# Kernel tuning notes

Measured on AMD Instinct MI355X. Metric: run time of the kernel, lower is better.

The kernel has to match this reference:

```python
import jax, jax.numpy as jnp
import numpy as np

B, Nq, C, H = 1, 300, 256, 8
h, w = 32, 32
HW = h * w
HID = 512  # rpe_hidden_dim
HD = C // H


def setup_inputs() -> dict:
    key = jax.random.key(0)
    ks = jax.random.split(key, 16)
    s = 0.02
    inp = {
        "raw_query": jax.random.normal(ks[0], (B, Nq, C), jnp.float32),
        "query_pos": jax.random.normal(ks[1], (B, Nq, C), jnp.float32),
        "reference_points": jax.random.uniform(ks[2], (B, Nq, 2), jnp.float32),
        "raw_src": jax.random.normal(ks[3], (B, HW, C), jnp.float32),
        "src_pos_embed": jax.random.normal(ks[4], (B, HW, C), jnp.float32),
        "Wq": jax.random.normal(ks[5], (C, C), jnp.float32) * s,
        "bq": jnp.zeros((C,), jnp.float32),
        "Wk": jax.random.normal(ks[6], (C, C), jnp.float32) * s,
        "bk": jnp.zeros((C,), jnp.float32),
        "Wv": jax.random.normal(ks[7], (C, C), jnp.float32) * s,
        "bv": jnp.zeros((C,), jnp.float32),
        "Wo": jax.random.normal(ks[8], (C, C), jnp.float32) * s,
        "bo": jnp.zeros((C,), jnp.float32),
        "W1": jax.random.normal(ks[9], (HID, 2), jnp.float32),   # cpb MLP layer 1
        "b1": jnp.zeros((HID,), jnp.float32),
        "W2": jax.random.normal(ks[10], (H, HID), jnp.float32) * s,  # cpb MLP layer 2 (no bias)
        "input_spatial_shapes": np.array([[h, w]], dtype=np.int64),
    }
    return inp


def _key_positions(hh, ww):
    ys = (jnp.arange(hh, dtype=jnp.float32) + 0.5) / hh
    xs = (jnp.arange(ww, dtype=jnp.float32) + 0.5) / ww
    yy, xx = jnp.meshgrid(ys, xs, indexing="ij")  # row-major: idx = y*w + x
    return jnp.stack([xx.ravel(), yy.ravel()], axis=-1)  # [HW, 2] (x, y)


def reference(raw_query, query_pos, reference_points, raw_src, src_pos_embed,
              Wq, bq, Wk, bk, Wv, bv, Wo, bo, W1, b1, W2, input_spatial_shapes):
    hh, ww = int(input_spatial_shapes[0, 0]), int(input_spatial_shapes[0, 1])
    scale = HD ** (-0.5)
    queries = raw_query + query_pos                      # [B,Nq,C]
    memory = raw_src + src_pos_embed                     # [B,HW,C]

    q = (queries @ Wq.T + bq).reshape(B, Nq, H, HD)
    k = (memory @ Wk.T + bk).reshape(B, hh * ww, H, HD)
    v = (memory @ Wv.T + bv).reshape(B, hh * ww, H, HD)

    logits = jnp.einsum("bqhd,bkhd->bhqk", q, k) * scale  # [B,H,Nq,HW]

    key_pos = _key_positions(hh, ww)                      # [HW,2]
    delta = reference_points[:, :, None, :] - key_pos[None, None]  # [B,Nq,HW,2]
    hid = jax.nn.relu(jnp.einsum("bqkc,hc->bqkh", delta, W1) + b1)  # [B,Nq,HW,HID]
    bias = jnp.einsum("bqkf,hf->bhqk", hid, W2)           # [B,H,Nq,HW]

    attn = jax.nn.softmax(logits + bias, axis=-1)
    out = jnp.einsum("bhqk,bkhd->bqhd", attn, v).reshape(B, Nq, C)
    return out @ Wo.T + bo
```

## Files before the change

### kernel.cpp

```cpp
#include <hip/hip_runtime.h>
#include <hip/hip_fp16.h>
#include <stdint.h>

#define NQ   300
#define CDIM 256
#define NH   8
#define HD   32
#define HWK  1024
#define HIDD 512

typedef __attribute__((ext_vector_type(8))) _Float16 f16x8;
typedef __attribute__((ext_vector_type(2))) _Float16 h2v;
typedef __attribute__((ext_vector_type(4))) float f32x4;

#define QB_OFF   0
#define KB_OFF   153600
#define VT_OFF   677888
#define PO_OFF   1202176
#define PL_OFF   3659776
#define A16_OFF  3736576
#define NX_OFF   4043776
#define NY_OFF   4044800
#define W2_OFF   4045824

__device__ __forceinline__ short f16b(float x){
  _Float16 h = (_Float16)x;
  return __builtin_bit_cast(short, h);
}

__device__ __forceinline__ uint32_t pk_f16(float a, float b){
  auto r = __builtin_amdgcn_cvt_pkrtz(a, b);
  return __builtin_bit_cast(uint32_t, r);
}

__global__ __launch_bounds__(256) void prep_kernel(
    const float* __restrict__ refp, const float* __restrict__ W1,
    const float* __restrict__ b1, const float* __restrict__ W2,
    short* __restrict__ a16, short* __restrict__ nx16,
    short* __restrict__ ny16, short* __restrict__ w216)
{
  int idx = blockIdx.x * 256 + threadIdx.x;
  if (idx < NQ*HIDD){
    int q = idx >> 9, f = idx & 511;
    float2 w = ((const float2*)W1)[f];
    float a = fmaf(w.x, refp[2*q], fmaf(w.y, refp[2*q+1], b1[f]));
    a16[idx] = f16b(a);
  } else {
    int j = idx - NQ*HIDD;
    if (j < HIDD){
      float2 w = ((const float2*)W1)[j];
      nx16[j] = f16b(-w.x);
      ny16[j] = f16b(-w.y);
    } else if (j < HIDD + NH*HIDD){
      int e = j - HIDD;
      w216[e] = f16b(W2[e]);
    }
  }
}

__global__ __launch_bounds__(256) void proj_kernel(
    const float* __restrict__ rq, const float* __restrict__ qp,
    const float* __restrict__ rs, const float* __restrict__ spe,
    const float* __restrict__ Wq, const float* __restrict__ bq,
    const float* __restrict__ Wk, const float* __restrict__ bk,
    const float* __restrict__ Wv, const float* __restrict__ bv,
    const float* __restrict__ Wo, const float* __restrict__ bo,
    char* __restrict__ ws, float* __restrict__ dout, int final_mode)
{
  int bxid = blockIdx.x;
  int tile = bxid >> 1, half = bxid & 1;
  const float *in1, *in2, *W, *bias;
  int r0, M, mode;
  const float* po = (const float*)(ws + PO_OFF);
  const float* pl = (const float*)(ws + PL_OFF);
  if (final_mode){
    in1 = po; in2 = nullptr; W = Wo; bias = bo;
    r0 = tile*16; M = NQ; mode = 3;
  } else if (tile < 19){
    in1 = rq; in2 = qp; W = Wq; bias = bq; r0 = tile*16; M = NQ; mode = 0;
  } else if (tile < 83){
    in1 = rs; in2 = spe; W = Wk; bias = bk; r0 = (tile-19)*16; M = HWK; mode = 1;
  } else {
    in1 = rs; in2 = spe; W = Wv; bias = bv; r0 = (tile-83)*16; M = HWK; mode = 2;
  }
  __shared__ __align__(16) float At[32][20];
  __shared__ float Wl[32][129];
  __shared__ float linv[16][8];
  int tid = threadIdx.x;
  int n_loc = tid & 127;
  int rg = tid >> 7;
  int n = half*128 + n_loc;
  float acc[8];
  float bv_ = bias[n];
  #pragma unroll
  for (int i=0;i<8;i++) acc[i] = bv_;

  if (mode == 3 && tid < 128){
    int r = tid >> 3, hh = tid & 7;
    int gr = r0 + r; if (gr >= M) gr = M - 1;
    float s = 0.f;
    #pragma unroll
    for (int p = 0; p < 8; p++) s += pl[((size_t)p*NQ+gr)*NH+hh];
    linv[r][hh] = 1.0f / s;
  }

  for (int c0 = 0; c0 < CDIM; c0 += 32){
    __syncthreads();
    for (int e = tid; e < 512; e += 256){
      int r = e >> 5, c = e & 31;
      int gr = r0 + r; if (gr >= M) gr = M - 1;
      float v;
      if (mode == 3){
        int cc = c0 + c;
        v = 0.f;
        #pragma unroll
        for (int p = 0; p < 8; p++) v += po[(size_t)(p*NQ+gr)*CDIM + cc];
        v *= linv[r][c0 >> 5];
      } else {
        v = in1[gr*CDIM + c0 + c];
        if (in2) v += in2[gr*CDIM + c0 + c];
      }
      At[c][r] = v;
    }
    for (int e = tid; e < 4096; e += 256){
      int c = e & 31, nn = e >> 5;
      Wl[c][nn] = W[(half*128 + nn)*CDIM + c0 + c];
    }
    __syncthreads();
    #pragma unroll
    for (int c = 0; c < 32; c++){
      float w = Wl[c][n_loc];
      const float4* ap = (const float4*)&At[c][rg*8];
      float4 a0 = ap[0], a1 = ap[1];
      acc[0] = fmaf(a0.x, w, acc[0]);
      acc[1] = fmaf(a0.y, w, acc[1]);
      acc[2] = fmaf(a0.z, w, acc[2]);
      acc[3] = fmaf(a0.w, w, acc[3]);
      acc[4] = fmaf(a1.x, w, acc[4]);
      acc[5] = fmaf(a1.y, w, acc[5]);
      acc[6] = fmaf(a1.z, w, acc[6]);
      acc[7] = fmaf(a1.w, w, acc[7]);
    }
  }

  if (mode == 0){
    short* qb = (short*)(ws + QB_OFF);
    const float s = 0.17677669529663687f;
    #pragma unroll
    for (int i=0;i<8;i++){
      int gr = r0 + rg*8 + i;
      if (gr < M) qb[gr*CDIM + n] = f16b(acc[i]*s);
    }
  } else if (mode == 1){
    short* kb = (short*)(ws + KB_OFF);
    int h = n >> 5, d = n & 31;
    #pragma unroll
    for (int i=0;i<8;i++){
      int gr = r0 + rg*8 + i;
      if (gr < M) kb[((size_t)h*HWK + gr)*HD + d] = f16b(acc[i]);
    }
  } else if (mode == 2){
    short* vt = (short*)(ws + VT_OFF);
    uint32_t p[4];
    #pragma unroll
    for (int i=0;i<4;i++) p[i] = pk_f16(acc[2*i], acc[2*i+1]);
    *(uint4*)(vt + n*HWK + r0 + rg*8) = make_uint4(p[0], p[1], p[2], p[3]);
  } else {
    #pragma unroll
    for (int i=0;i<8;i++){
      int gr = r0 + rg*8 + i;
      if (gr < M) dout[gr*CDIM + n] = acc[i];
    }
  }
}

__global__ __launch_bounds__(256, 5) void fused_kernel(
    const short* __restrict__ a16, const short* __restrict__ nx16,
    const short* __restrict__ ny16, const short* __restrict__ w216,
    const short* __restrict__ qb, const short* __restrict__ kb,
    const short* __restrict__ vt, float* __restrict__ po,
    float* __restrict__ pl)
{
  int bid = blockIdx.x;
  int q = bid >> 3, kr = bid & 7;
  int tid = threadIdx.x, wave = tid >> 6, lane = tid & 63;
  int n = lane & 15, qd = lane >> 4;

  __shared__ __align__(16) _Float16 nwx[HIDD];
  __shared__ __align__(16) _Float16 c1s[4][HIDD];
  __shared__ __align__(16) _Float16 w2l[NH][520];
  __shared__ __align__(16) _Float16 pb[NH][136];
  __shared__ __align__(16) float part[4][NH][32];
  __shared__ float lsum[4][NH];

  {
    int f0 = tid * 2;
    h2v a2 = *(const h2v*)(a16 + q*HIDD + f0);
    h2v ny2 = *(const h2v*)(ny16 + f0);
    h2v nx2 = *(const h2v*)(nx16 + f0);
    *(h2v*)&nwx[f0] = nx2;
    #pragma unroll
    for (int r = 0; r < 4; r++){
      _Float16 kyh = (_Float16)(((float)(kr*4 + r) + 0.5f) * (1.0f/32.0f));
      h2v ky2 = {kyh, kyh};
      *(h2v*)&c1s[r][f0] = ny2 * ky2 + a2;
    }
  }
  for (int e = tid; e < 512; e += 256){
    int r = e >> 6, c = e & 63;
    *(f16x8*)&w2l[r][c*8] = *(const f16x8*)(w216 + r*HIDD + c*8);
  }
  f16x8 qfrag;
  if (n < NH) qfrag = *(const f16x8*)(qb + q*CDIM + n*HD + qd*8);
  else { f16x8 z = {0,0,0,0,0,0,0,0}; qfrag = z; }
  f16x8 qm[NH];
  #pragma unroll
  for (int h = 0; h < NH; h++){
    f16x8 z = {0,0,0,0,0,0,0,0};
    qm[h] = (n == h) ? qfrag : z;
  }
  __syncthreads();

  const int kyrow = kr*4 + wave;
  const int kbase = kyrow * 32;

  f32x4 acc[2];
  #pragma unroll
  for (int t = 0; t < 2; t++){
    int k0 = kbase + t*16;
    f32x4 d = {0.f,0.f,0.f,0.f};
    #pragma unroll
    for (int h = 0; h < NH; h++){
      f16x8 af = *(const f16x8*)(kb + ((size_t)h*HWK + k0 + n)*HD + qd*8);
      d = __builtin_amdgcn_mfma_f32_16x16x32_f16(af, qm[h], d, 0, 0, 0);
    }
    acc[t] = d;
  }

  _Float16 kxAh = (_Float16)(((float)n + 0.5f) * (1.0f/32.0f));
  _Float16 kxBh = (_Float16)(((float)n + 16.5f) * (1.0f/32.0f));
  f16x8 kxA8, kxB8, z8;
  #pragma unroll
  for (int j = 0; j < 8; j++){ kxA8[j] = kxAh; kxB8[j] = kxBh; z8[j] = (_Float16)0.f; }
  const _Float16* c1r = &c1s[wave][0];
  #pragma unroll 4
  for (int kc = 0; kc < 16; kc++){
    int f0 = kc*32 + qd*8;
    f16x8 c1v = *(const f16x8*)(c1r + f0);
    f16x8 wxv = *(const f16x8*)(&nwx[f0]);
    f16x8 bfr = *(const f16x8*)(&w2l[n & 7][f0]);
    #pragma unroll
    for (int t = 0; t < 2; t++){
      f16x8 kx8 = t ? kxB8 : kxA8;
      f16x8 e = __builtin_elementwise_max(wxv * kx8 + c1v, z8);
      acc[t] = __builtin_amdgcn_mfma_f32_16x16x32_f16(e, bfr, acc[t], 0, 0, 0);
    }
  }

  float lacc = 0.f;
  #pragma unroll
  for (int t = 0; t < 2; t++){
    float e0 = __expf(acc[t][0]);
    float e1 = __expf(acc[t][1]);
    float e2 = __expf(acc[t][2]);
    float e3 = __expf(acc[t][3]);
    if (n < NH){
      uint2 p2;
      p2.x = pk_f16(e0, e1);
      p2.y = pk_f16(e2, e3);
      *(uint2*)&pb[n][wave*32 + t*16 + qd*4] = p2;
    }
    float s = e0 + e1 + e2 + e3;
    s += __shfl_xor(s, 16);
    s += __shfl_xor(s, 32);
    lacc += s;
  }
  if (lane < NH) lsum[wave][lane] = lacc;

  #pragma unroll
  for (int h = 0; h < NH; h++){
    int kl = wave*32 + qd*8;
    f16x8 pa = *(const f16x8*)&pb[h][kl];
    f16x8 v0 = *(const f16x8*)(vt + ((size_t)(h*HD +      n))*HWK + kr*128 + kl);
    f16x8 v1 = *(const f16x8*)(vt + ((size_t)(h*HD + 16 + n))*HWK + kr*128 + kl);
    f32x4 o0 = {0.f,0.f,0.f,0.f}, o1 = {0.f,0.f,0.f,0.f};
    o0 = __builtin_amdgcn_mfma_f32_16x16x32_f16(pa, v0, o0, 0, 0, 0);
    o1 = __builtin_amdgcn_mfma_f32_16x16x32_f16(pa, v1, o1, 0, 0, 0);
    if (qd == 0){
      part[wave][h][n]      = o0[0];
      part[wave][h][16 + n] = o1[0];
    }
  }
  __syncthreads();

  {
    int h = tid >> 5, d = tid & 31;
    float s = part[0][h][d] + part[1][h][d] + part[2][h][d] + part[3][h][d];
    po[((size_t)kr*NQ + q)*CDIM + tid] = s;
    if (tid < NH)
      pl[((size_t)kr*NQ + q)*NH + tid] =
          lsum[0][tid] + lsum[1][tid] + lsum[2][tid] + lsum[3][tid];
  }
}

extern "C" void kernel_launch(void* const* d_in, const int* in_sizes, int n_in,
                              void* d_out, int out_size, void* d_ws, size_t ws_size,
                              hipStream_t stream)
{
  const float* rq  = (const float*)d_in[0];
  const float* qp  = (const float*)d_in[1];
  const float* rp  = (const float*)d_in[2];
  const float* rs  = (const float*)d_in[3];
  const float* spe = (const float*)d_in[4];
  const float* Wq  = (const float*)d_in[5];
  const float* bq  = (const float*)d_in[6];
  const float* Wk  = (const float*)d_in[7];
  const float* bk  = (const float*)d_in[8];
  const float* Wv  = (const float*)d_in[9];
  const float* bv  = (const float*)d_in[10];
  const float* Wo  = (const float*)d_in[11];
  const float* bo  = (const float*)d_in[12];
  const float* W1  = (const float*)d_in[13];
  const float* b1  = (const float*)d_in[14];
  const float* W2  = (const float*)d_in[15];
  char* ws = (char*)d_ws;
  float* dout = (float*)d_out;

  prep_kernel<<<618, 256, 0, stream>>>(rp, W1, b1, W2,
      (short*)(ws + A16_OFF), (short*)(ws + NX_OFF),
      (short*)(ws + NY_OFF), (short*)(ws + W2_OFF));
  proj_kernel<<<294, 256, 0, stream>>>(rq, qp, rs, spe, Wq, bq, Wk, bk,
      Wv, bv, Wo, bo, ws, dout, 0);
  fused_kernel<<<2400, 256, 0, stream>>>((const short*)(ws + A16_OFF),
      (const short*)(ws + NX_OFF), (const short*)(ws + NY_OFF),
      (const short*)(ws + W2_OFF), (const short*)(ws + QB_OFF),
      (const short*)(ws + KB_OFF), (const short*)(ws + VT_OFF),
      (float*)(ws + PO_OFF), (float*)(ws + PL_OFF));
  proj_kernel<<<38, 256, 0, stream>>>(rq, qp, rs, spe, Wq, bq, Wk, bk,
      Wv, bv, Wo, bo, ws, dout, 1);
}
```

Measured before the change: 167.1 us.

## Merge prep into projection kernel, precompute masked Q tiles, raise fused occupancy

The separate prep launch is folded into the projection kernel as extra blocks, removing one launch and its serialization. The projection is retiled into quarters of 64 output columns, giving more blocks. The Q projection now also writes a zero-padded per-head masked Q layout, so the fused kernel loads ready-made MFMA B fragments instead of building eight masked copies in registers. The fused kernel shares one LDS buffer between c1s and part and raises launch bounds to 8 blocks per CU. The trade-off is extra global writes for the zeroed Q tiles and more register pressure under the higher occupancy target.

New measurement: 171.9 us. 2.9% more time.

```diff
diff --git a/kernel.cpp b/kernel.cpp
--- a/kernel.cpp
+++ b/kernel.cpp
@@ -22,6 +22,7 @@
 #define NX_OFF   4043776
 #define NY_OFF   4044800
 #define W2_OFF   4045824
+#define QZ_OFF   4054016
 
 __device__ __forceinline__ short f16b(float x){
   _Float16 h = (_Float16)x;
@@ -33,29 +34,9 @@
   return __builtin_bit_cast(uint32_t, r);
 }
 
-__global__ __launch_bounds__(256) void prep_kernel(
-    const float* __restrict__ refp, const float* __restrict__ W1,
-    const float* __restrict__ b1, const float* __restrict__ W2,
-    short* __restrict__ a16, short* __restrict__ nx16,
-    short* __restrict__ ny16, short* __restrict__ w216)
-{
-  int idx = blockIdx.x * 256 + threadIdx.x;
-  if (idx < NQ*HIDD){
-    int q = idx >> 9, f = idx & 511;
-    float2 w = ((const float2*)W1)[f];
-    float a = fmaf(w.x, refp[2*q], fmaf(w.y, refp[2*q+1], b1[f]));
-    a16[idx] = f16b(a);
-  } else {
-    int j = idx - NQ*HIDD;
-    if (j < HIDD){
-      float2 w = ((const float2*)W1)[j];
-      nx16[j] = f16b(-w.x);
-      ny16[j] = f16b(-w.y);
-    } else if (j < HIDD + NH*HIDD){
-      int e = j - HIDD;
-      w216[e] = f16b(W2[e]);
-    }
-  }
+__device__ __forceinline__ h2v cvt2h(float a, float b){
+  auto r = __builtin_amdgcn_cvt_pkrtz(a, b);
+  return __builtin_bit_cast(h2v, r);
 }
 
 __global__ __launch_bounds__(256) void proj_kernel(
@@ -64,25 +45,247 @@
     const float* __restrict__ Wq, const float* __restrict__ bq,
     const float* __restrict__ Wk, const float* __restrict__ bk,
     const float* __restrict__ Wv, const float* __restrict__ bv,
-    const float* __restrict__ Wo, const float* __restrict__ bo,
-    char* __restrict__ ws, float* __restrict__ dout, int final_mode)
+    const float* __restrict__ refp, const float* __restrict__ W1,
+    const float* __restrict__ b1, const float* __restrict__ W2,
+    char* __restrict__ ws)
 {
   int bxid = blockIdx.x;
-  int tile = bxid >> 1, half = bxid & 1;
+  int tid = threadIdx.x;
+
+  if (bxid >= 588){
+    int pidx = (bxid - 588)*256 + tid;
+    if (pidx < 153600){
+      int q = pidx >> 9, f = pidx & 511;
+      float2 w = ((const float2*)W1)[f];
+      float a = fmaf(w.x, refp[2*q], fmaf(w.y, refp[2*q+1], b1[f]));
+      ((short*)(ws + A16_OFF))[pidx] = f16b(a);
+    } else if (pidx < 154112){
+      int f = pidx - 153600;
+      float2 w = ((const float2*)W1)[f];
+      ((short*)(ws + NX_OFF))[f] = f16b(-w.x);
+      ((short*)(ws + NY_OFF))[f] = f16b(-w.y);
+    } else if (pidx < 158208){
+      int e = pidx - 154112;
+      ((short*)(ws + W2_OFF))[e] = f16b(W2[e]);
+    } else if (pidx < 302208){
+      int z = pidx - 158208;
+      int g = z >> 2, p = z & 3;
+      int q = g / 120, r = g - q*120;
+      int h = r / 15,  m = r - h*15;
+      int n = m + (m >= h ? 1 : 0);
+      f16x8 z8 = {0,0,0,0,0,0,0,0};
+      *(f16x8*)((short*)(ws + QZ_OFF) + (((q*NH + h)*16 + n) << 5) + p*8) = z8;
+    }
+    return;
+  }
+
+  int tile = bxid >> 2, quarter = bxid & 3;
   const float *in1, *in2, *W, *bias;
   int r0, M, mode;
-  const float* po = (const float*)(ws + PO_OFF);
-  const float* pl = (const float*)(ws + PL_OFF);
-  if (final_mode){
-    in1 = po; in2 = nullptr; W = Wo; bias = bo;
-    r0 = tile*16; M = NQ; mode = 3;
-  } else if (tile < 19){
+  if (tile < 19){
     in1 = rq; in2 = qp; W = Wq; bias = bq; r0 = tile*16; M = NQ; mode = 0;
   } else if (tile < 83){
     in1 = rs; in2 = spe; W = Wk; bias = bk; r0 = (tile-19)*16; M = HWK; mode = 1;
   } else {
     in1 = rs; in2 = spe; W = Wv; bias = bv; r0 = (tile-83)*16; M = HWK; mode = 2;
   }
+  __shared__ __align__(16) float At[32][20];
+  __shared__ float Wl[32][68];
+  int nq = tid & 63;
+  int rg = tid >> 6;
+  int n = quarter*64 + nq;
+  float acc[4];
+  float bv_ = bias[n];
+  #pragma unroll
+  for (int i=0;i<4;i++) acc[i] = bv_;
+
+  for (int c0 = 0; c0 < CDIM; c0 += 32){
+    __syncthreads();
+    for (int e = tid; e < 512; e += 256){
+      int r = e >> 5, c = e & 31;
+      int gr = r0 + r; if (gr >= M) gr = M - 1;
+      float v = in1[gr*CDIM + c0 + c];
+      if (in2) v += in2[gr*CDIM + c0 + c];
+      At[c][r] = v;
+    }
+    for (int e = tid; e < 2048; e += 256){
+      int c = e & 31, nn = e >> 5;
+      Wl[c][nn] = W[(quarter*64 + nn)*CDIM + c0 + c];
+    }
+    __syncthreads();
+    #pragma unroll
+    for (int c = 0; c < 32; c++){
+      float w = Wl[c][nq];
+      float4 a = *(const float4*)&At[c][rg*4];
+      acc[0] = fmaf(a.x, w, acc[0]);
+      acc[1] = fmaf(a.y, w, acc[1]);
+      acc[2] = fmaf(a.z, w, acc[2]);
+      acc[3] = fmaf(a.w, w, acc[3]);
+    }
+  }
+
+  if (mode == 0){
+    short* qb = (short*)(ws + QB_OFF);
+    short* qz = (short*)(ws + QZ_OFF);
+    const float s = 0.17677669529663687f;
+    int h = n >> 5, d = n & 31;
+    #pragma unroll
+    for (int i=0;i<4;i++){
+      int gr = r0 + rg*4 + i;
+      if (gr < M){
+        short v = f16b(acc[i]*s);
+        qb[gr*CDIM + n] = v;
+        qz[(((gr*NH + h)*16 + h) << 5) + d] = v;
+      }
+    }
+  } else if (mode == 1){
+    short* kb = (short*)(ws + KB_OFF);
+    int h = n >> 5, d = n & 31;
+    #pragma unroll
+    for (int i=0;i<4;i++){
+      int gr = r0 + rg*4 + i;
+      if (gr < M) kb[((size_t)h*HWK + gr)*HD + d] = f16b(acc[i]);
+    }
+  } else {
+    short* vt = (short*)(ws + VT_OFF);
+    uint2 p2;
+    p2.x = pk_f16(acc[0], acc[1]);
+    p2.y = pk_f16(acc[2], acc[3]);
+    *(uint2*)(vt + n*HWK + r0 + rg*4) = p2;
+  }
+}
+
+__global__ __launch_bounds__(256, 8) void fused_kernel(
+    const short* __restrict__ a16, const short* __restrict__ nx16,
+    const short* __restrict__ ny16, const short* __restrict__ w216,
+    const short* __restrict__ qz, const short* __restrict__ kb,
+    const short* __restrict__ vt, float* __restrict__ po,
+    float* __restrict__ pl)
+{
+  int bid = blockIdx.x;
+  int q = bid >> 3, kr = bid & 7;
+  int tid = threadIdx.x, wave = tid >> 6, lane = tid & 63;
+  int n = lane & 15, qd = lane >> 4;
+
+  __shared__ __align__(16) _Float16 nwx[HIDD];
+  __shared__ __align__(16) char pool[4096];
+  __shared__ __align__(16) _Float16 w2l[NH][520];
+  __shared__ __align__(16) _Float16 pb[NH][136];
+  __shared__ float lsum[4][NH];
+  _Float16 (*c1s)[HIDD] = (_Float16 (*)[HIDD])pool;
+  float (*part)[NH][32] = (float (*)[NH][32])pool;
+
+  {
+    int f0 = tid * 2;
+    h2v a2  = *(const h2v*)(a16 + q*HIDD + f0);
+    h2v ny2 = *(const h2v*)(ny16 + f0);
+    h2v nx2 = *(const h2v*)(nx16 + f0);
+    *(h2v*)&nwx[f0] = nx2;
+    #pragma unroll
+    for (int r = 0; r < 4; r++){
+      _Float16 kyh = (_Float16)(((float)(kr*4 + r) + 0.5f) * (1.0f/32.0f));
+      h2v ky2 = {kyh, kyh};
+      *(h2v*)&c1s[r][f0] = ny2 * ky2 + a2;
+    }
+  }
+  for (int e = tid; e < 512; e += 256){
+    int r = e >> 6, c = e & 63;
+    *(f16x8*)&w2l[r][c*8] = *(const f16x8*)(w216 + r*HIDD + c*8);
+  }
+  __syncthreads();
+
+  const int kyrow = kr*4 + wave;
+  const int kbase = kyrow * 32;
+
+  const short* qzq = qz + q*(NH*16*32);
+  int loff = (n << 5) + qd*8;
+  f32x4 acc[2] = {{0.f,0.f,0.f,0.f},{0.f,0.f,0.f,0.f}};
+  #pragma unroll
+  for (int h = 0; h < NH; h++){
+    f16x8 bq_ = *(const f16x8*)(qzq + (h << 9) + loff);
+    #pragma unroll
+    for (int t = 0; t < 2; t++){
+      int k0 = kbase + t*16;
+      f16x8 af = *(const f16x8*)(kb + ((size_t)h*HWK + k0 + n)*HD + qd*8);
+      acc[t] = __builtin_amdgcn_mfma_f32_16x16x32_f16(af, bq_, acc[t], 0, 0, 0);
+    }
+  }
+
+  _Float16 kxAh = (_Float16)(((float)n + 0.5f) * (1.0f/32.0f));
+  _Float16 kxBh = (_Float16)(((float)n + 16.5f) * (1.0f/32.0f));
+  f16x8 kxA8, kxB8, z8;
+  #pragma unroll
+  for (int j = 0; j < 8; j++){ kxA8[j] = kxAh; kxB8[j] = kxBh; z8[j] = (_Float16)0.f; }
+  const _Float16* c1r = &c1s[wave][0];
+  #pragma unroll 4
+  for (int kc = 0; kc < 16; kc++){
+    int f0 = kc*32 + qd*8;
+    f16x8 c1v = *(const f16x8*)(c1r + f0);
+    f16x8 wxv = *(const f16x8*)(&nwx[f0]);
+    f16x8 bfr = *(const f16x8*)(&w2l[n & 7][f0]);
+    #pragma unroll
+    for (int t = 0; t < 2; t++){
+      f16x8 kx8 = t ? kxB8 : kxA8;
+      f16x8 e = __builtin_elementwise_max(wxv * kx8 + c1v, z8);
+      acc[t] = __builtin_amdgcn_mfma_f32_16x16x32_f16(e, bfr, acc[t], 0, 0, 0);
+    }
+  }
+
+  float lacc = 0.f;
+  #pragma unroll
+  for (int t = 0; t < 2; t++){
+    float e0 = __expf(acc[t][0]);
+    float e1 = __expf(acc[t][1]);
+    float e2 = __expf(acc[t][2]);
+    float e3 = __expf(acc[t][3]);
+    if (n < NH){
+      uint2 p2;
+      p2.x = pk_f16(e0, e1);
+      p2.y = pk_f16(e2, e3);
+      *(uint2*)&pb[n][wave*32 + t*16 + qd*4] = p2;
+    }
+    float s = e0 + e1 + e2 + e3;
+    s += __shfl_xor(s, 16);
+    s += __shfl_xor(s, 32);
+    lacc += s;
+  }
+  if (lane < NH) lsum[wave][lane] = lacc;
+
+  #pragma unroll
+  for (int h = 0; h < NH; h++){
+    int kl = wave*32 + qd*8;
+    f16x8 pa = *(const f16x8*)&pb[h][kl];
+    f16x8 v0 = *(const f16x8*)(vt + ((size_t)(h*HD +      n))*HWK + kr*128 + kl);
+    f16x8 v1 = *(const f16x8*)(vt + ((size_t)(h*HD + 16 + n))*HWK + kr*128 + kl);
+    f32x4 o0 = {0.f,0.f,0.f,0.f}, o1 = {0.f,0.f,0.f,0.f};
+    o0 = __builtin_amdgcn_mfma_f32_16x16x32_f16(pa, v0, o0, 0, 0, 0);
+    o1 = __builtin_amdgcn_mfma_f32_16x16x32_f16(pa, v1, o1, 0, 0, 0);
+    if (qd == 0){
+      part[wave][h][n]      = o0[0];
+      part[wave][h][16 + n] = o1[0];
+    }
+  }
+  __syncthreads();
+
+  {
+    int h = tid >> 5, d = tid & 31;
+    float s = part[0][h][d] + part[1][h][d] + part[2][h][d] + part[3][h][d];
+    po[((size_t)kr*NQ + q)*CDIM + tid] = s;
+    if (tid < NH)
+      pl[((size_t)kr*NQ + q)*NH + tid] =
+          lsum[0][tid] + lsum[1][tid] + lsum[2][tid] + lsum[3][tid];
+  }
+}
+
+__global__ __launch_bounds__(256) void projf_kernel(
+    const float* __restrict__ Wo, const float* __restrict__ bo,
+    char* __restrict__ ws, float* __restrict__ dout)
+{
+  int bxid = blockIdx.x;
+  int tile = bxid >> 1, half = bxid & 1;
+  const float* po = (const float*)(ws + PO_OFF);
+  const float* pl = (const float*)(ws + PL_OFF);
+  int r0 = tile*16, M = NQ;
   __shared__ __align__(16) float At[32][20];
   __shared__ float Wl[32][129];
   __shared__ float linv[16][8];
@@ -91,11 +294,11 @@
   int rg = tid >> 7;
   int n = half*128 + n_loc;
   float acc[8];
-  float bv_ = bias[n];
+  float bv_ = bo[n];
   #pragma unroll
   for (int i=0;i<8;i++) acc[i] = bv_;
 
-  if (mode == 3 && tid < 128){
+  if (tid < 128){
     int r = tid >> 3, hh = tid & 7;
     int gr = r0 + r; if (gr >= M) gr = M - 1;
     float s = 0.f;
@@ -109,22 +312,15 @@
     for (int e = tid; e < 512; e += 256){
       int r = e >> 5, c = e & 31;
       int gr = r0 + r; if (gr >= M) gr = M - 1;
-      float v;
-      if (mode == 3){
-        int cc = c0 + c;
-        v = 0.f;
-        #pragma unroll
-        for (int p = 0; p < 8; p++) v += po[(size_t)(p*NQ+gr)*CDIM + cc];
-        v *= linv[r][c0 >> 5];
-      } else {
-        v = in1[gr*CDIM + c0 + c];
-        if (in2) v += in2[gr*CDIM + c0 + c];
-      }
-      At[c][r] = v;
+      int cc = c0 + c;
+      float v = 0.f;
+      #pragma unroll
+      for (int p = 0; p < 8; p++) v += po[(size_t)(p*NQ+gr)*CDIM + cc];
+      At[c][r] = v * linv[r][c0 >> 5];
     }
     for (int e = tid; e < 4096; e += 256){
       int c = e & 31, nn = e >> 5;
-      Wl[c][nn] = W[(half*128 + nn)*CDIM + c0 + c];
+      Wl[c][nn] = Wo[(half*128 + nn)*CDIM + c0 + c];
     }
     __syncthreads();
     #pragma unroll
@@ -142,164 +338,10 @@
       acc[7] = fmaf(a1.w, w, acc[7]);
     }
   }
-
-  if (mode == 0){
-    short* qb = (short*)(ws + QB_OFF);
-    const float s = 0.17677669529663687f;
-    #pragma unroll
-    for (int i=0;i<8;i++){
-      int gr = r0 + rg*8 + i;
-      if (gr < M) qb[gr*CDIM + n] = f16b(acc[i]*s);
-    }
-  } else if (mode == 1){
-    short* kb = (short*)(ws + KB_OFF);
-    int h = n >> 5, d = n & 31;
-    #pragma unroll
-    for (int i=0;i<8;i++){
-      int gr = r0 + rg*8 + i;
-      if (gr < M) kb[((size_t)h*HWK + gr)*HD + d] = f16b(acc[i]);
-    }
-  } else if (mode == 2){
-    short* vt = (short*)(ws + VT_OFF);
-    uint32_t p[4];
-    #pragma unroll
-    for (int i=0;i<4;i++) p[i] = pk_f16(acc[2*i], acc[2*i+1]);
-    *(uint4*)(vt + n*HWK + r0 + rg*8) = make_uint4(p[0], p[1], p[2], p[3]);
-  } else {
-    #pragma unroll
-    for (int i=0;i<8;i++){
-      int gr = r0 + rg*8 + i;
-      if (gr < M) dout[gr*CDIM + n] = acc[i];
-    }
-  }
-}
-
-__global__ __launch_bounds__(256, 5) void fused_kernel(
-    const short* __restrict__ a16, const short* __restrict__ nx16,
-    const short* __restrict__ ny16, const short* __restrict__ w216,
-    const short* __restrict__ qb, const short* __restrict__ kb,
-    const short* __restrict__ vt, float* __restrict__ po,
-    float* __restrict__ pl)
-{
-  int bid = blockIdx.x;
-  int q = bid >> 3, kr = bid & 7;
-  int tid = threadIdx.x, wave = tid >> 6, lane = tid & 63;
-  int n = lane & 15, qd = lane >> 4;
-
-  __shared__ __align__(16) _Float16 nwx[HIDD];
-  __shared__ __align__(16) _Float16 c1s[4][HIDD];
-  __shared__ __align__(16) _Float16 w2l[NH][520];
-  __shared__ __align__(16) _Float16 pb[NH][136];
-  __shared__ __align__(16) float part[4][NH][32];
-  __shared__ float lsum[4][NH];
-
-  {
-    int f0 = tid * 2;
-    h2v a2 = *(const h2v*)(a16 + q*HIDD + f0);
-    h2v ny2 = *(const h2v*)(ny16 + f0);
-    h2v nx2 = *(const h2v*)(nx16 + f0);
-    *(h2v*)&nwx[f0] = nx2;
-    #pragma unroll
-    for (int r = 0; r < 4; r++){
-      _Float16 kyh = (_Float16)(((float)(kr*4 + r) + 0.5f) * (1.0f/32.0f));
-      h2v ky2 = {kyh, kyh};
-      *(h2v*)&c1s[r][f0] = ny2 * ky2 + a2;
-    }
-  }
-  for (int e = tid; e < 512; e += 256){
-    int r = e >> 6, c = e & 63;
-    *(f16x8*)&w2l[r][c*8] = *(const f16x8*)(w216 + r*HIDD + c*8);
-  }
-  f16x8 qfrag;
-  if (n < NH) qfrag = *(const f16x8*)(qb + q*CDIM + n*HD + qd*8);
-  else { f16x8 z = {0,0,0,0,0,0,0,0}; qfrag = z; }
-  f16x8 qm[NH];
-  #pragma unroll
-  for (int h = 0; h < NH; h++){
-    f16x8 z = {0,0,0,0,0,0,0,0};
-    qm[h] = (n == h) ? qfrag : z;
-  }
-  __syncthreads();
-
-  const int kyrow = kr*4 + wave;
-  const int kbase = kyrow * 32;
-
-  f32x4 acc[2];
-  #pragma unroll
-  for (int t = 0; t < 2; t++){
-    int k0 = kbase + t*16;
-    f32x4 d = {0.f,0.f,0.f,0.f};
-    #pragma unroll
-    for (int h = 0; h < NH; h++){
-      f16x8 af = *(const f16x8*)(kb + ((size_t)h*HWK + k0 + n)*HD + qd*8);
-      d = __builtin_amdgcn_mfma_f32_16x16x32_f16(af, qm[h], d, 0, 0, 0);
-    }
-    acc[t] = d;
-  }
-
-  _Float16 kxAh = (_Float16)(((float)n + 0.5f) * (1.0f/32.0f));
-  _Float16 kxBh = (_Float16)(((float)n + 16.5f) * (1.0f/32.0f));
-  f16x8 kxA8, kxB8, z8;
-  #pragma unroll
-  for (int j = 0; j < 8; j++){ kxA8[j] = kxAh; kxB8[j] = kxBh; z8[j] = (_Float16)0.f; }
-  const _Float16* c1r = &c1s[wave][0];
-  #pragma unroll 4
-  for (int kc = 0; kc < 16; kc++){
-    int f0 = kc*32 + qd*8;
-    f16x8 c1v = *(const f16x8*)(c1r + f0);
-    f16x8 wxv = *(const f16x8*)(&nwx[f0]);
-    f16x8 bfr = *(const f16x8*)(&w2l[n & 7][f0]);
-    #pragma unroll
-    for (int t = 0; t < 2; t++){
-      f16x8 kx8 = t ? kxB8 : kxA8;
-      f16x8 e = __builtin_elementwise_max(wxv * kx8 + c1v, z8);
-      acc[t] = __builtin_amdgcn_mfma_f32_16x16x32_f16(e, bfr, acc[t], 0, 0, 0);
-    }
-  }
-
-  float lacc = 0.f;
-  #pragma unroll
-  for (int t = 0; t < 2; t++){
-    float e0 = __expf(acc[t][0]);
-    float e1 = __expf(acc[t][1]);
-    float e2 = __expf(acc[t][2]);
-    float e3 = __expf(acc[t][3]);
-    if (n < NH){
-      uint2 p2;
-      p2.x = pk_f16(e0, e1);
-      p2.y = pk_f16(e2, e3);
-      *(uint2*)&pb[n][wave*32 + t*16 + qd*4] = p2;
-    }
-    float s = e0 + e1 + e2 + e3;
-    s += __shfl_xor(s, 16);
-    s += __shfl_xor(s, 32);
-    lacc += s;
-  }
-  if (lane < NH) lsum[wave][lane] = lacc;
-
-  #pragma unroll
-  for (int h = 0; h < NH; h++){
-    int kl = wave*32 + qd*8;
-    f16x8 pa = *(const f16x8*)&pb[h][kl];
-    f16x8 v0 = *(const f16x8*)(vt + ((size_t)(h*HD +      n))*HWK + kr*128 + kl);
-    f16x8 v1 = *(const f16x8*)(vt + ((size_t)(h*HD + 16 + n))*HWK + kr*128 + kl);
-    f32x4 o0 = {0.f,0.f,0.f,0.f}, o1 = {0.f,0.f,0.f,0.f};
-    o0 = __builtin_amdgcn_mfma_f32_16x16x32_f16(pa, v0, o0, 0, 0, 0);
-    o1 = __builtin_amdgcn_mfma_f32_16x16x32_f16(pa, v1, o1, 0, 0, 0);
-    if (qd == 0){
-      part[wave][h][n]      = o0[0];
-      part[wave][h][16 + n] = o1[0];
-    }
-  }
-  __syncthreads();
-
-  {
-    int h = tid >> 5, d = tid & 31;
-    float s = part[0][h][d] + part[1][h][d] + part[2][h][d] + part[3][h][d];
-    po[((size_t)kr*NQ + q)*CDIM + tid] = s;
-    if (tid < NH)
-      pl[((size_t)kr*NQ + q)*NH + tid] =
-          lsum[0][tid] + lsum[1][tid] + lsum[2][tid] + lsum[3][tid];
+  #pragma unroll
+  for (int i=0;i<8;i++){
+    int gr = r0 + rg*8 + i;
+    if (gr < M) dout[gr*CDIM + n] = acc[i];
   }
 }
 
@@ -326,16 +368,12 @@
   char* ws = (char*)d_ws;
   float* dout = (float*)d_out;
 
-  prep_kernel<<<618, 256, 0, stream>>>(rp, W1, b1, W2,
-      (short*)(ws + A16_OFF), (short*)(ws + NX_OFF),
-      (short*)(ws + NY_OFF), (short*)(ws + W2_OFF));
-  proj_kernel<<<294, 256, 0, stream>>>(rq, qp, rs, spe, Wq, bq, Wk, bk,
-      Wv, bv, Wo, bo, ws, dout, 0);
+  proj_kernel<<<1769, 256, 0, stream>>>(rq, qp, rs, spe, Wq, bq, Wk, bk,
+      Wv, bv, rp, W1, b1, W2, ws);
   fused_kernel<<<2400, 256, 0, stream>>>((const short*)(ws + A16_OFF),
       (const short*)(ws + NX_OFF), (const short*)(ws + NY_OFF),
-      (const short*)(ws + W2_OFF), (const short*)(ws + QB_OFF),
+      (const short*)(ws + W2_OFF), (const short*)(ws + QZ_OFF),
       (const short*)(ws + KB_OFF), (const short*)(ws + VT_OFF),
       (float*)(ws + PO_OFF), (float*)(ws + PL_OFF));
-  proj_kernel<<<38, 256, 0, stream>>>(rq, qp, rs, spe, Wq, bq, Wk, bk,
-      Wv, bv, Wo, bo, ws, dout, 1);
-}
+  projf_kernel<<<38, 256, 0, stream>>>(Wo, bo, ws, dout);
+}
```

## Process two queries per block to fill idle MFMA columns and reuse K/V loads

Applied to the files above, without the earlier changes.

Each fused_kernel block now handles two queries instead of one, halving the grid. The 16 MFMA columns, of which only 8 were used for heads before, now hold both queries' heads, so the logit and P·V MFMAs and their K/V/W2 loads are shared across two queries. The bias-MLP MFMAs are duplicated per query, and the launch-bounds occupancy hint drops from 5 to 4. Shared memory is pooled by aliasing c1s with part, which is safe because each wave overwrites only its own slice.

New measurement: 154.5 us. 7.5% less time.

```diff
diff --git a/kernel.cpp b/kernel.cpp
--- a/kernel.cpp
+++ b/kernel.cpp
@@ -31,6 +31,11 @@
 __device__ __forceinline__ uint32_t pk_f16(float a, float b){
   auto r = __builtin_amdgcn_cvt_pkrtz(a, b);
   return __builtin_bit_cast(uint32_t, r);
+}
+
+__device__ __forceinline__ h2v cvt2h(float a, float b){
+  auto r = __builtin_amdgcn_cvt_pkrtz(a, b);
+  return __builtin_bit_cast(h2v, r);
 }
 
 __global__ __launch_bounds__(256) void prep_kernel(
@@ -174,7 +179,7 @@
   }
 }
 
-__global__ __launch_bounds__(256, 5) void fused_kernel(
+__global__ __launch_bounds__(256, 4) void fused_kernel(
     const short* __restrict__ a16, const short* __restrict__ nx16,
     const short* __restrict__ ny16, const short* __restrict__ w216,
     const short* __restrict__ qb, const short* __restrict__ kb,
@@ -182,59 +187,59 @@
     float* __restrict__ pl)
 {
   int bid = blockIdx.x;
-  int q = bid >> 3, kr = bid & 7;
+  int q0 = (bid >> 3) * 2, kr = bid & 7;
   int tid = threadIdx.x, wave = tid >> 6, lane = tid & 63;
   int n = lane & 15, qd = lane >> 4;
 
   __shared__ __align__(16) _Float16 nwx[HIDD];
-  __shared__ __align__(16) _Float16 c1s[4][HIDD];
+  __shared__ __align__(16) char pool[8192];
   __shared__ __align__(16) _Float16 w2l[NH][520];
-  __shared__ __align__(16) _Float16 pb[NH][136];
-  __shared__ __align__(16) float part[4][NH][32];
-  __shared__ float lsum[4][NH];
+  __shared__ __align__(16) _Float16 pb[2][NH][136];
+  __shared__ float lsum[4][16];
+  _Float16 (*c1s)[4][HIDD] = (_Float16 (*)[4][HIDD])pool;
+  float (*part)[4][NH][32] = (float (*)[4][NH][32])pool;
 
   {
     int f0 = tid * 2;
-    h2v a2 = *(const h2v*)(a16 + q*HIDD + f0);
     h2v ny2 = *(const h2v*)(ny16 + f0);
     h2v nx2 = *(const h2v*)(nx16 + f0);
     *(h2v*)&nwx[f0] = nx2;
     #pragma unroll
-    for (int r = 0; r < 4; r++){
-      _Float16 kyh = (_Float16)(((float)(kr*4 + r) + 0.5f) * (1.0f/32.0f));
-      h2v ky2 = {kyh, kyh};
-      *(h2v*)&c1s[r][f0] = ny2 * ky2 + a2;
+    for (int qq = 0; qq < 2; qq++){
+      h2v a2 = *(const h2v*)(a16 + (q0+qq)*HIDD + f0);
+      #pragma unroll
+      for (int r = 0; r < 4; r++){
+        _Float16 kyh = (_Float16)(((float)(kr*4 + r) + 0.5f) * (1.0f/32.0f));
+        h2v ky2 = {kyh, kyh};
+        *(h2v*)&c1s[qq][r][f0] = ny2 * ky2 + a2;
+      }
     }
   }
   for (int e = tid; e < 512; e += 256){
     int r = e >> 6, c = e & 63;
     *(f16x8*)&w2l[r][c*8] = *(const f16x8*)(w216 + r*HIDD + c*8);
   }
-  f16x8 qfrag;
-  if (n < NH) qfrag = *(const f16x8*)(qb + q*CDIM + n*HD + qd*8);
-  else { f16x8 z = {0,0,0,0,0,0,0,0}; qfrag = z; }
+  f16x8 qfrag = *(const f16x8*)(qb + (q0 + (n >> 3))*CDIM + (n & 7)*HD + qd*8);
   f16x8 qm[NH];
   #pragma unroll
   for (int h = 0; h < NH; h++){
     f16x8 z = {0,0,0,0,0,0,0,0};
-    qm[h] = (n == h) ? qfrag : z;
+    qm[h] = ((n & 7) == h) ? qfrag : z;
   }
   __syncthreads();
 
   const int kyrow = kr*4 + wave;
   const int kbase = kyrow * 32;
 
-  f32x4 acc[2];
+  f32x4 acc1[2] = {{0.f,0.f,0.f,0.f},{0.f,0.f,0.f,0.f}};
   #pragma unroll
   for (int t = 0; t < 2; t++){
     int k0 = kbase + t*16;
-    f32x4 d = {0.f,0.f,0.f,0.f};
     #pragma unroll
     for (int h = 0; h < NH; h++){
       f16x8 af = *(const f16x8*)(kb + ((size_t)h*HWK + k0 + n)*HD + qd*8);
-      d = __builtin_amdgcn_mfma_f32_16x16x32_f16(af, qm[h], d, 0, 0, 0);
-    }
-    acc[t] = d;
+      acc1[t] = __builtin_amdgcn_mfma_f32_16x16x32_f16(af, qm[h], acc1[t], 0, 0, 0);
+    }
   }
 
   _Float16 kxAh = (_Float16)(((float)n + 0.5f) * (1.0f/32.0f));
@@ -242,64 +247,78 @@
   f16x8 kxA8, kxB8, z8;
   #pragma unroll
   for (int j = 0; j < 8; j++){ kxA8[j] = kxAh; kxB8[j] = kxBh; z8[j] = (_Float16)0.f; }
-  const _Float16* c1r = &c1s[wave][0];
+  f32x4 accb[2][2];
+  accb[0][0] = acc1[0]; accb[0][1] = acc1[1];
+  accb[1][0] = acc1[0]; accb[1][1] = acc1[1];
+  const _Float16* c1r0 = &c1s[0][wave][0];
+  const _Float16* c1r1 = &c1s[1][wave][0];
   #pragma unroll 4
   for (int kc = 0; kc < 16; kc++){
     int f0 = kc*32 + qd*8;
-    f16x8 c1v = *(const f16x8*)(c1r + f0);
+    f16x8 c10 = *(const f16x8*)(c1r0 + f0);
+    f16x8 c11 = *(const f16x8*)(c1r1 + f0);
     f16x8 wxv = *(const f16x8*)(&nwx[f0]);
     f16x8 bfr = *(const f16x8*)(&w2l[n & 7][f0]);
     #pragma unroll
     for (int t = 0; t < 2; t++){
       f16x8 kx8 = t ? kxB8 : kxA8;
-      f16x8 e = __builtin_elementwise_max(wxv * kx8 + c1v, z8);
-      acc[t] = __builtin_amdgcn_mfma_f32_16x16x32_f16(e, bfr, acc[t], 0, 0, 0);
-    }
-  }
-
+      f16x8 e0 = __builtin_elementwise_max(wxv * kx8 + c10, z8);
+      accb[0][t] = __builtin_amdgcn_mfma_f32_16x16x32_f16(e0, bfr, accb[0][t], 0, 0, 0);
+      f16x8 e1 = __builtin_elementwise_max(wxv * kx8 + c11, z8);
+      accb[1][t] = __builtin_amdgcn_mfma_f32_16x16x32_f16(e1, bfr, accb[1][t], 0, 0, 0);
+    }
+  }
+
+  int qsel = n >> 3, hsel = n & 7;
   float lacc = 0.f;
   #pragma unroll
   for (int t = 0; t < 2; t++){
-    float e0 = __expf(acc[t][0]);
-    float e1 = __expf(acc[t][1]);
-    float e2 = __expf(acc[t][2]);
-    float e3 = __expf(acc[t][3]);
-    if (n < NH){
-      uint2 p2;
-      p2.x = pk_f16(e0, e1);
-      p2.y = pk_f16(e2, e3);
-      *(uint2*)&pb[n][wave*32 + t*16 + qd*4] = p2;
-    }
+    f32x4 a = qsel ? accb[1][t] : accb[0][t];
+    float e0 = __expf(a[0]);
+    float e1 = __expf(a[1]);
+    float e2 = __expf(a[2]);
+    float e3 = __expf(a[3]);
+    uint2 p2;
+    p2.x = pk_f16(e0, e1);
+    p2.y = pk_f16(e2, e3);
+    *(uint2*)&pb[qsel][hsel][wave*32 + t*16 + qd*4] = p2;
     float s = e0 + e1 + e2 + e3;
     s += __shfl_xor(s, 16);
     s += __shfl_xor(s, 32);
     lacc += s;
   }
-  if (lane < NH) lsum[wave][lane] = lacc;
+  if (lane < 16) lsum[wave][lane] = lacc;
 
   #pragma unroll
   for (int h = 0; h < NH; h++){
     int kl = wave*32 + qd*8;
-    f16x8 pa = *(const f16x8*)&pb[h][kl];
+    f16x8 pa = *(const f16x8*)&pb[n & 1][h][kl];
     f16x8 v0 = *(const f16x8*)(vt + ((size_t)(h*HD +      n))*HWK + kr*128 + kl);
     f16x8 v1 = *(const f16x8*)(vt + ((size_t)(h*HD + 16 + n))*HWK + kr*128 + kl);
     f32x4 o0 = {0.f,0.f,0.f,0.f}, o1 = {0.f,0.f,0.f,0.f};
     o0 = __builtin_amdgcn_mfma_f32_16x16x32_f16(pa, v0, o0, 0, 0, 0);
     o1 = __builtin_amdgcn_mfma_f32_16x16x32_f16(pa, v1, o1, 0, 0, 0);
     if (qd == 0){
-      part[wave][h][n]      = o0[0];
-      part[wave][h][16 + n] = o1[0];
+      part[0][wave][h][n]      = o0[0];
+      part[1][wave][h][n]      = o0[1];
+      part[0][wave][h][16 + n] = o1[0];
+      part[1][wave][h][16 + n] = o1[1];
     }
   }
   __syncthreads();
 
   {
     int h = tid >> 5, d = tid & 31;
-    float s = part[0][h][d] + part[1][h][d] + part[2][h][d] + part[3][h][d];
-    po[((size_t)kr*NQ + q)*CDIM + tid] = s;
-    if (tid < NH)
-      pl[((size_t)kr*NQ + q)*NH + tid] =
-          lsum[0][tid] + lsum[1][tid] + lsum[2][tid] + lsum[3][tid];
+    #pragma unroll
+    for (int qq = 0; qq < 2; qq++){
+      float s = part[qq][0][h][d] + part[qq][1][h][d]
+              + part[qq][2][h][d] + part[qq][3][h][d];
+      po[((size_t)kr*NQ + q0 + qq)*CDIM + tid] = s;
+    }
+    if (tid < 16){
+      float s = lsum[0][tid] + lsum[1][tid] + lsum[2][tid] + lsum[3][tid];
+      pl[((size_t)kr*NQ + q0 + (tid >> 3))*NH + (tid & 7)] = s;
+    }
   }
 }
 
@@ -331,7 +350,7 @@
       (short*)(ws + NY_OFF), (short*)(ws + W2_OFF));
   proj_kernel<<<294, 256, 0, stream>>>(rq, qp, rs, spe, Wq, bq, Wk, bk,
       Wv, bv, Wo, bo, ws, dout, 0);
-  fused_kernel<<<2400, 256, 0, stream>>>((const short*)(ws + A16_OFF),
+  fused_kernel<<<1200, 256, 0, stream>>>((const short*)(ws + A16_OFF),
       (const short*)(ws + NX_OFF), (const short*)(ws + NY_OFF),
       (const short*)(ws + W2_OFF), (const short*)(ws + QB_OFF),
       (const short*)(ws + KB_OFF), (const short*)(ws + VT_OFF),
```
